# Kernel optimization log

Measured on AMD Instinct MI355X. Metric: run time of the kernel, lower is better.

Reference implementation:

```python
import jax, jax.numpy as jnp
import numpy as np

B, L, D, H = 2, 2048, 1024, 16
HD = D // H
EPS = 1e-6

def _rms(x, w):
    return x * jax.lax.rsqrt(jnp.mean(x * x, axis=-1, keepdims=True) + EPS) * w

def _lin(x, w, b=None):
    y = x @ w.T
    return y if b is None else y + b

def setup_inputs() -> dict:
    key = jax.random.key(0)
    ks = jax.random.split(key, 16)
    def w(i, shape, s=0.02):
        return jax.random.normal(ks[i], shape, dtype=jnp.float32) * s
    return dict(
        z=jax.random.normal(ks[0], (B, L, D), dtype=jnp.float32),
        connection=jax.random.normal(ks[1], (B, L, D), dtype=jnp.float32),
        w_z=jnp.ones(D, jnp.float32), w_c=jnp.ones(D, jnp.float32), w_mlp=jnp.ones(D, jnp.float32),
        f_w1=w(2, (2 * D, D)), f_b1=jnp.zeros(2 * D, jnp.float32),
        f_w2=w(3, (D, 2 * D)), f_b2=jnp.zeros(D, jnp.float32),
        g_w1=w(4, (D, 2 * D)), g_b1=jnp.zeros(D, jnp.float32),
        g_w2=w(5, (D, D)), g_b2=jnp.zeros(D, jnp.float32),
        dt=jnp.float32(0.1),
        q_w=w(6, (D, 2 * D)), k_w=w(7, (D, 2 * D)), v_w=w(8, (D, D)), o_w=w(9, (D, D)),
        temp=jnp.float32(1.0),
        cu_w1=w(10, (2 * D, 3 * D)), cu_b1=jnp.zeros(2 * D, jnp.float32),
        cu_w2=w(11, (D, 2 * D)), cu_b2=jnp.zeros(D, jnp.float32),
        m_w1=w(12, (4 * D, D)), m_b1=jnp.zeros(4 * D, jnp.float32),
        m_w2=w(13, (D, 4 * D)), m_b2=jnp.zeros(D, jnp.float32),
    )

def reference(z, connection, w_z, w_c, w_mlp,
              f_w1, f_b1, f_w2, f_b2, g_w1, g_b1, g_w2, g_b2, dt,
              q_w, k_w, v_w, o_w, temp,
              cu_w1, cu_b1, cu_w2, cu_b2,
              m_w1, m_b1, m_w2, m_b2):
    z_before = z
    zn = _rms(z, w_z)
    cn = _rms(connection, w_c)

    # covariant vector field: dz = dt * (F(zn) + gamma(cat(cn, F(zn))))
    dz_local = _lin(jax.nn.silu(_lin(zn, f_w1, f_b1)), f_w2, f_b2)
    corr = _lin(jnp.tanh(_lin(jnp.concatenate([cn, dz_local], -1), g_w1, g_b1)), g_w2, g_b2)
    dz = dt * (dz_local + corr)

    # covariant sigmoid attention
    zc = jnp.concatenate([zn, cn], -1)                       # [B,L,2D]
    Q = _lin(zc, q_w).reshape(B, L, H, HD).transpose(0, 2, 1, 3)  # bhld
    K = _lin(zc, k_w).reshape(B, L, H, HD).transpose(0, 2, 1, 3)
    V = _lin(zn, v_w).reshape(B, L, H, HD).transpose(0, 2, 1, 3)
    scores = jnp.einsum('bhld,bhmd->bhlm', Q, K) * (HD ** -0.5) * temp
    rel = jax.nn.sigmoid(scores)
    rel_sum = jnp.clip(jnp.sum(rel, -1, keepdims=True), 1.0, None)
    attn = jnp.einsum('bhlm,bhmd->bhld', rel, V) / rel_sum
    ctx = _lin(attn.transpose(0, 2, 1, 3).reshape(B, L, D), o_w)

    z1 = z + dz + ctx

    # connection update
    delta = _lin(jax.nn.silu(_lin(jnp.concatenate([connection, z1, dz], -1), cu_w1, cu_b1)), cu_w2, cu_b2)
    conn_new = connection + delta

    # MLP block
    z2 = z1 + _lin(jax.nn.silu(_lin(_rms(z1, w_mlp), m_w1, m_b1)), m_w2, m_b2)
    return (z2, conn_new, z_before)
```

## Files before the change

kernel.cpp:

```cpp
#include <hip/hip_runtime.h>


typedef unsigned short u16;
typedef __attribute__((ext_vector_type(8))) short short8;
typedef __attribute__((ext_vector_type(8))) unsigned short us8;
typedef __attribute__((ext_vector_type(4))) float f32x4;
typedef __attribute__((ext_vector_type(4))) unsigned short us4;
typedef __attribute__((ext_vector_type(2))) unsigned int u32x2;

__device__ __forceinline__ float b2f(u16 u) {
    union { unsigned u; float f; } c; c.u = ((unsigned)u) << 16; return c.f;
}
__device__ __forceinline__ u16 f2b(float f) {
    union { float f; unsigned u; } c; c.f = f;
    unsigned x = c.u;
    unsigned r = (x + 0x7fffu + ((x >> 16) & 1u)) >> 16;
    return (u16)r;
}
__device__ __forceinline__ float fast_rcp(float x) {
    return __builtin_amdgcn_rcpf(x);
}
__device__ __forceinline__ unsigned cvt_pk_bf16(float a, float b) {
    unsigned r;
    asm("v_cvt_pk_bf16_f32 %0, %1, %2" : "=v"(r) : "v"(a), "v"(b));
    return r;
}

__device__ __forceinline__ void async_copy16(const u16* g, u16* l) {
    __builtin_amdgcn_global_load_lds(
        (const __attribute__((address_space(1))) unsigned int*)(g),
        (__attribute__((address_space(3))) unsigned int*)(l), 16, 0, 0);
}

__global__ __launch_bounds__(256) void cvt_k(const float* __restrict__ s,
                                             u16* __restrict__ d, int n) {
    int i = (blockIdx.x * 256 + threadIdx.x) * 4;
    if (i >= n) return;
    f32x4 v = *(const f32x4*)(s + i);
    us4 o;
#pragma unroll
    for (int k = 0; k < 4; k++) o[k] = f2b(v[k]);
    *(us4*)(d + i) = o;
}

__global__ __launch_bounds__(256) void rmsf_k(const float* __restrict__ x,
                                              const float* __restrict__ w,
                                              u16* __restrict__ y,
                                              float* __restrict__ cp, int D) {
    int n = blockIdx.x;
    const float* xr = x + (size_t)n * D;
    int i0 = threadIdx.x << 2;
    f32x4 v = *(const f32x4*)(xr + i0);
    if (cp) *(f32x4*)(cp + (size_t)n * D + i0) = v;
    float s = v[0] * v[0] + v[1] * v[1] + v[2] * v[2] + v[3] * v[3];
#pragma unroll
    for (int m = 32; m >= 1; m >>= 1) s += __shfl_xor(s, m, 64);
    __shared__ float red[4];
    if ((threadIdx.x & 63) == 0) red[threadIdx.x >> 6] = s;
    __syncthreads();
    float tot = red[0] + red[1] + red[2] + red[3];
    float scale = rsqrtf(tot / (float)D + 1e-6f);
    f32x4 wv = *(const f32x4*)(w + i0);
    us4 o;
#pragma unroll
    for (int k = 0; k < 4; k++) o[k] = f2b(v[k] * scale * wv[k]);
    *(us4*)(y + (size_t)n * D + i0) = o;
}

__global__ __launch_bounds__(256) void rmsb_k(const u16* __restrict__ x,
                                              const float* __restrict__ w,
                                              u16* __restrict__ y, int D) {
    int n = blockIdx.x;
    const u16* xr = x + (size_t)n * D;
    int i0 = threadIdx.x << 2;
    us4 xv = *(const us4*)(xr + i0);
    float v[4]; float s = 0.f;
#pragma unroll
    for (int k = 0; k < 4; k++) { v[k] = b2f(xv[k]); s += v[k] * v[k]; }
#pragma unroll
    for (int m = 32; m >= 1; m >>= 1) s += __shfl_xor(s, m, 64);
    __shared__ float red[4];
    if ((threadIdx.x & 63) == 0) red[threadIdx.x >> 6] = s;
    __syncthreads();
    float tot = red[0] + red[1] + red[2] + red[3];
    float scale = rsqrtf(tot / (float)D + 1e-6f);
    f32x4 wv = *(const f32x4*)(w + i0);
    us4 o;
#pragma unroll
    for (int k = 0; k < 4; k++) o[k] = f2b(v[k] * scale * wv[k]);
    *(us4*)(y + (size_t)n * D + i0) = o;
}

template <int BN, int NSEG>
__global__ __launch_bounds__(256) void gemm_t(const u16* __restrict__ A0,
                                              const u16* __restrict__ A1,
                                              const u16* __restrict__ A2,
                                              const u16* __restrict__ W,
                                              const float* __restrict__ bias,
                                              u16* __restrict__ C,
                                              int K, int O, int act, int mode) {
    constexpr int NJ = BN / 32;
    constexpr int WN = BN / 2;
    __shared__ u16 Asm[2][128 * 64];
    __shared__ u16 Bsm[2][BN * 64];

    const int tid = threadIdx.x;
    const int wid = tid >> 6, lane = tid & 63;
    const int l15 = lane & 15, quad = lane >> 4;
    const int lsw = l15 & 7;
    const int row0 = blockIdx.y * 128, col0 = blockIdx.x * BN;
    const int wm = (wid >> 1) << 6, wn = (wid & 1) * WN;

    const int rb = tid >> 3;
    const int gg = ((tid & 7) ^ (rb & 7)) << 3;
    const int sA = (NSEG == 1) ? K : 1024;
    const size_t aoff = (size_t)(row0 + rb) * sA + gg;
    const size_t boff = (size_t)(col0 + rb) * K + gg;
    const int ldsb = wid << 9;

    f32x4 acc[4][NJ];
#pragma unroll
    for (int i = 0; i < 4; i++)
#pragma unroll
        for (int j = 0; j < NJ; j++) acc[i][j] = (f32x4){0.f, 0.f, 0.f, 0.f};

    auto stage = [&](int buf, int kof) {
        const u16* Ab; int kcol;
        if constexpr (NSEG == 1) { Ab = A0; kcol = kof; }
        else {
            int seg = kof >> 10;
            Ab = (seg == 0) ? A0 : ((NSEG == 3 && seg == 2) ? A2 : A1);
            kcol = kof & 1023;
        }
        const u16* as = Ab + aoff + kcol;
        const u16* bs = W + boff + kof;
#pragma unroll
        for (int i = 0; i < 4; i++)
            async_copy16(as + (size_t)(32 * i) * sA, &Asm[buf][(i << 11) + ldsb]);
#pragma unroll
        for (int i = 0; i < BN / 32; i++)
            async_copy16(bs + (size_t)(32 * i) * K, &Bsm[buf][(i << 11) + ldsb]);
    };

    const int nk = K >> 6;
    stage(0, 0);
    __syncthreads();
    for (int kk = 0; kk < nk; kk++) {
        int cur = kk & 1;
        if (kk + 1 < nk) stage(1 - cur, (kk + 1) << 6);
        const u16* Ab = Asm[cur];
        const u16* Bb = Bsm[cur];
#pragma unroll
        for (int h = 0; h < 2; h++) {
            const int gq = (((h << 2) + quad) ^ lsw) << 3;
            short8 af[4], bf[NJ];
#pragma unroll
            for (int i = 0; i < 4; i++)
                af[i] = *(const short8*)&Ab[(wm + i * 16 + l15) * 64 + gq];
#pragma unroll
            for (int j = 0; j < NJ; j++)
                bf[j] = *(const short8*)&Bb[(wn + j * 16 + l15) * 64 + gq];
#pragma unroll
            for (int i = 0; i < 4; i++)
#pragma unroll
                for (int j = 0; j < NJ; j++)
                    acc[i][j] = __builtin_amdgcn_mfma_f32_16x16x32_bf16(af[i], bf[j], acc[i][j], 0, 0, 0);
        }
        __syncthreads();
    }

    if (mode == 0) {
#pragma unroll
        for (int j = 0; j < NJ; j++) {
            int col = col0 + wn + j * 16 + l15;
            float bb = bias ? bias[col] : 0.f;
#pragma unroll
            for (int i = 0; i < 4; i++) {
                int rowb = row0 + wm + i * 16 + (quad << 2);
#pragma unroll
                for (int g = 0; g < 4; g++) {
                    float v = acc[i][j][g] + bb;
                    if (act == 1) {
                        v = v * fast_rcp(1.f + __expf(-v));
                    } else if (act == 2) {
                        float t = __expf(v * 2.f);
                        v = 1.f - 2.f * fast_rcp(1.f + t);
                    }
                    C[(size_t)(rowb + g) * O + col] = f2b(v);
                }
            }
        }
    } else {
#pragma unroll
        for (int j = 0; j < NJ; j++) {
            int col = col0 + wn + j * 16 + l15;
            int h = col >> 6, d = col & 63;
#pragma unroll
            for (int i = 0; i < 4; i++) {
                int rowb = row0 + wm + i * 16 + (quad << 2);
                int bb_ = rowb >> 11;
                int tok = rowb & 2047;
                us4 pk;
#pragma unroll
                for (int g = 0; g < 4; g++) pk[g] = f2b(acc[i][j][g]);
                *(us4*)&C[(size_t)(((bb_ << 4) + h) * 64 + d) * 2048 + tok] = pk;
            }
        }
    }
}

__global__ __launch_bounds__(256) void attn_k(const u16* __restrict__ QK,
                                              const u16* __restrict__ VT,
                                              const float* __restrict__ temp_p,
                                              u16* __restrict__ Oa) {
    const int L = 2048, D = 1024, SQ = 2048;
    __shared__ u16 Ks[2][64 * 64];
    __shared__ u16 Vs[2][64 * 64];
    __shared__ u16 plds[4][16 * 72];

    const int tid = threadIdx.x;
    const int w = tid >> 6, lane = tid & 63;
    const int l15 = lane & 15, quad = lane >> 4;
    const int bh = blockIdx.x >> 4;
    const int qb0 = (blockIdx.x & 15) << 7;
    const int b = bh >> 4, h = bh & 15;
    const float nsc2 = -0.125f * temp_p[0] * 1.44269504f;

    short8 aq[2][2];
#pragma unroll
    for (int qt = 0; qt < 2; qt++) {
        size_t row = (size_t)(b * L + qb0 + w * 32 + qt * 16 + l15) * SQ + h * 64;
#pragma unroll
        for (int hf = 0; hf < 2; hf++)
            aq[qt][hf] = *(const short8*)(QK + row + hf * 32 + quad * 8);
    }

    const u16* Kbase = QK + 1024 + (size_t)(b * L) * SQ + h * 64;
    const u16* VTb   = VT + (size_t)bh * 64 * L;

    const int i0 = tid, i1 = tid + 256;
    const int r0 = i0 >> 3, g0 = (i0 & 7) ^ (r0 & 7);
    const int r1 = i1 >> 3, g1 = (i1 & 7) ^ (r1 & 7);
    const u16* kS0 = Kbase + (size_t)r0 * SQ + g0 * 8;
    const u16* kS1 = Kbase + (size_t)r1 * SQ + g1 * 8;
    const u16* vS0 = VTb + (size_t)r0 * L + g0 * 8;
    const u16* vS1 = VTb + (size_t)r1 * L + g1 * 8;

    auto stage = [&](int buf, int mc) {
        async_copy16(kS0 + (size_t)mc * SQ, &Ks[buf][w << 9]);
        async_copy16(kS1 + (size_t)mc * SQ, &Ks[buf][2048 + (w << 9)]);
        async_copy16(vS0 + mc, &Vs[buf][w << 9]);
        async_copy16(vS1 + mc, &Vs[buf][2048 + (w << 9)]);
    };

    f32x4 acc[2][4];
#pragma unroll
    for (int i = 0; i < 2; i++)
#pragma unroll
        for (int j = 0; j < 4; j++) acc[i][j] = (f32x4){0.f, 0.f, 0.f, 0.f};
    float rs[2] = {0.f, 0.f};
    u16* P = plds[w];
    const int lsw = l15 & 7;

    stage(0, 0);
    __syncthreads();
    for (int it = 0; it < 32; it++) {
        int cur = it & 1;
        if (it < 31) stage(1 - cur, (it + 1) << 6);
        const u16* Kt = Ks[cur];
        const u16* Vt = Vs[cur];
#pragma unroll
        for (int qt = 0; qt < 2; qt++) {
#pragma unroll
            for (int ks = 0; ks < 4; ks++) {
                f32x4 s = (f32x4){0.f, 0.f, 0.f, 0.f};
#pragma unroll
                for (int hf = 0; hf < 2; hf++) {
                    int slot = ((ks * 16 + l15) * 8 + ((hf * 4 + quad) ^ lsw)) * 8;
                    short8 bk = *(const short8*)&Kt[slot];
                    s = __builtin_amdgcn_mfma_f32_16x16x32_bf16(bk, aq[qt][hf], s, 0, 0, 0);
                }
                float p0 = fast_rcp(1.f + __builtin_amdgcn_exp2f(s[0] * nsc2));
                float p1 = fast_rcp(1.f + __builtin_amdgcn_exp2f(s[1] * nsc2));
                float p2 = fast_rcp(1.f + __builtin_amdgcn_exp2f(s[2] * nsc2));
                float p3 = fast_rcp(1.f + __builtin_amdgcn_exp2f(s[3] * nsc2));
                rs[qt] += (p0 + p1) + (p2 + p3);
                u32x2 pk2;
                pk2[0] = cvt_pk_bf16(p0, p1);
                pk2[1] = cvt_pk_bf16(p2, p3);
                *(u32x2*)&P[l15 * 72 + ks * 16 + (quad << 2)] = pk2;
            }
#pragma unroll
            for (int kh = 0; kh < 2; kh++) {
                short8 ap = *(const short8*)&P[l15 * 72 + kh * 32 + quad * 8];
#pragma unroll
                for (int dt = 0; dt < 4; dt++) {
                    int slot = ((dt * 16 + l15) * 8 + ((kh * 4 + quad) ^ lsw)) * 8;
                    short8 bv = *(const short8*)&Vt[slot];
                    acc[qt][dt] = __builtin_amdgcn_mfma_f32_16x16x32_bf16(ap, bv, acc[qt][dt], 0, 0, 0);
                }
            }
        }
        __syncthreads();
    }

#pragma unroll
    for (int qt = 0; qt < 2; qt++) {
        rs[qt] += __shfl_xor(rs[qt], 16, 64);
        rs[qt] += __shfl_xor(rs[qt], 32, 64);
    }

#pragma unroll
    for (int qt = 0; qt < 2; qt++) {
        u16* orow = Oa + (size_t)(b * L + qb0 + w * 32 + qt * 16) * D + h * 64;
#pragma unroll
        for (int g = 0; g < 4; g++) {
            int row = quad * 4 + g;
            float denom = __shfl(rs[qt], row, 64);
            float rd = fast_rcp(fmaxf(denom, 1.0f));
#pragma unroll
            for (int dt = 0; dt < 4; dt++)
                orow[(size_t)row * D + dt * 16 + l15] = f2b(acc[qt][dt][g] * rd);
        }
    }
}

__global__ void dz_k(u16* __restrict__ d, const u16* __restrict__ a,
                     const u16* __restrict__ b, const float* __restrict__ dtp, int n) {
    int i = (blockIdx.x * 256 + threadIdx.x) * 8;
    if (i >= n) return;
    float dt = dtp[0];
    us8 va = *(const us8*)(a + i), vb = *(const us8*)(b + i);
    us8 o;
#pragma unroll
    for (int k = 0; k < 8; k++) o[k] = f2b(dt * (b2f(va[k]) + b2f(vb[k])));
    *(us8*)(d + i) = o;
}

__global__ void z1_k(u16* __restrict__ d, const float* __restrict__ z,
                     const u16* __restrict__ dz, const u16* __restrict__ ctx, int n) {
    int i = (blockIdx.x * 256 + threadIdx.x) * 8;
    if (i >= n) return;
    f32x4 z0 = *(const f32x4*)(z + i), z4 = *(const f32x4*)(z + i + 4);
    us8 vd = *(const us8*)(dz + i), vc = *(const us8*)(ctx + i);
    us8 o;
#pragma unroll
    for (int k = 0; k < 4; k++) {
        o[k]     = f2b(z0[k] + b2f(vd[k])     + b2f(vc[k]));
        o[k + 4] = f2b(z4[k] + b2f(vd[k + 4]) + b2f(vc[k + 4]));
    }
    *(us8*)(d + i) = o;
}

__global__ void connew_k(float* __restrict__ d, const float* __restrict__ conn,
                         const u16* __restrict__ delta, int n) {
    int i = (blockIdx.x * 256 + threadIdx.x) * 8;
    if (i >= n) return;
    f32x4 c0 = *(const f32x4*)(conn + i), c4 = *(const f32x4*)(conn + i + 4);
    us8 vd = *(const us8*)(delta + i);
    f32x4 o0, o4;
#pragma unroll
    for (int k = 0; k < 4; k++) {
        o0[k] = c0[k] + b2f(vd[k]);
        o4[k] = c4[k] + b2f(vd[k + 4]);
    }
    *(f32x4*)(d + i) = o0;
    *(f32x4*)(d + i + 4) = o4;
}

__global__ void z2_k(float* __restrict__ d, const u16* __restrict__ z1,
                     const u16* __restrict__ mf, int n) {
    int i = (blockIdx.x * 256 + threadIdx.x) * 8;
    if (i >= n) return;
    us8 va = *(const us8*)(z1 + i), vb = *(const us8*)(mf + i);
    f32x4 o0, o4;
#pragma unroll
    for (int k = 0; k < 4; k++) {
        o0[k] = b2f(va[k]) + b2f(vb[k]);
        o4[k] = b2f(va[k + 4]) + b2f(vb[k + 4]);
    }
    *(f32x4*)(d + i) = o0;
    *(f32x4*)(d + i + 4) = o4;
}

extern "C" void kernel_launch(void* const* d_in, const int* in_sizes, int n_in,
                              void* d_out, int out_size, void* d_ws, size_t ws_size,
                              hipStream_t stream) {
    const int B = 2, L = 2048, D = 1024, H = 16, N = B * L;
    const float* z      = (const float*)d_in[0];
    const float* conn   = (const float*)d_in[1];
    const float* w_z    = (const float*)d_in[2];
    const float* w_c    = (const float*)d_in[3];
    const float* w_mlp  = (const float*)d_in[4];
    const float* f_w1   = (const float*)d_in[5];
    const float* f_b1   = (const float*)d_in[6];
    const float* f_w2   = (const float*)d_in[7];
    const float* f_b2   = (const float*)d_in[8];
    const float* g_w1   = (const float*)d_in[9];
    const float* g_b1   = (const float*)d_in[10];
    const float* g_w2   = (const float*)d_in[11];
    const float* g_b2   = (const float*)d_in[12];
    const float* dt_p   = (const float*)d_in[13];
    const float* q_w    = (const float*)d_in[14];
    const float* k_w    = (const float*)d_in[15];
    const float* v_w    = (const float*)d_in[16];
    const float* o_w    = (const float*)d_in[17];
    const float* temp_p = (const float*)d_in[18];
    const float* cu_w1  = (const float*)d_in[19];
    const float* cu_b1  = (const float*)d_in[20];
    const float* cu_w2  = (const float*)d_in[21];
    const float* cu_b2  = (const float*)d_in[22];
    const float* m_w1   = (const float*)d_in[23];
    const float* m_b1   = (const float*)d_in[24];
    const float* m_w2   = (const float*)d_in[25];
    const float* m_b2   = (const float*)d_in[26];

    float* out = (float*)d_out;
    u16* ws  = (u16*)d_ws;
    const size_t U = (size_t)N * D;

    u16* zn    = ws + 0 * U;
    u16* cn    = ws + 1 * U;
    u16* h1    = ws + 2 * U;
    u16* dzl   = ws + 4 * U;
    u16* gh    = ws + 5 * U;
    u16* corr  = ws + 6 * U;
    u16* dz    = ws + 7 * U;
    u16* connb = ws + 8 * U;
    u16* QK    = ws + 2 * U;
    u16* VT    = ws + 4 * U;
    u16* attnb = ws + 1 * U;
    u16* ctx   = ws + 4 * U;
    u16* z1    = ws + 5 * U;
    u16* cu_h  = ws + 2 * U;
    u16* delta = ws + 1 * U;
    u16* z1n   = ws + 0 * U;
    u16* mh    = ws + 1 * U;
    u16* mf    = ws + 6 * U;

    u16* wb = ws + 9 * U;
    u16* bf_w1  = wb + 0;
    u16* bf_w2  = wb + 2 * 1024 * 1024;
    u16* bg_w1  = wb + 4 * 1024 * 1024;
    u16* bg_w2  = wb + 6 * 1024 * 1024;
    u16* bqk_w  = wb + 7 * 1024 * 1024;
    u16* bv_w   = wb + 11 * 1024 * 1024;
    u16* bo_w   = wb + 12 * 1024 * 1024;
    u16* bcu_w1 = wb + 13 * 1024 * 1024;
    u16* bcu_w2 = wb + 19 * 1024 * 1024;
    u16* bm_w1  = wb + 21 * 1024 * 1024;
    u16* bm_w2  = wb + 25 * 1024 * 1024;

    auto cvt = [&](const float* s, u16* d, int n) {
        cvt_k<<<n / 1024, 256, 0, stream>>>(s, d, n);
    };
    cvt(f_w1, bf_w1, 2 * D * D);   cvt(f_w2, bf_w2, 2 * D * D);
    cvt(g_w1, bg_w1, 2 * D * D);   cvt(g_w2, bg_w2, D * D);
    cvt(q_w, bqk_w, 2 * D * D);    cvt(k_w, bqk_w + 2 * D * D, 2 * D * D);
    cvt(v_w, bv_w, D * D);         cvt(o_w, bo_w, D * D);
    cvt(cu_w1, bcu_w1, 6 * D * D); cvt(cu_w2, bcu_w2, 2 * D * D);
    cvt(m_w1, bm_w1, 4 * D * D);   cvt(m_w2, bm_w2, 4 * D * D);
    cvt(conn, connb, N * D);

    const int EW8 = (N * D / 8 + 255) / 256;
    auto gemm = [&](const u16* A, const u16* W, const float* bias, u16* C,
                    int K, int O, int act, int mode = 0) {
        if (O == 1024) {
            dim3 grid(16, 32);
            gemm_t<64, 1><<<grid, 256, 0, stream>>>(A, nullptr, nullptr, W, bias, C, K, O, act, mode);
        } else {
            dim3 grid(O / 128, 32);
            gemm_t<128, 1><<<grid, 256, 0, stream>>>(A, nullptr, nullptr, W, bias, C, K, O, act, mode);
        }
    };

    rmsf_k<<<N, 256, 0, stream>>>(z, w_z, zn, out + 2 * U, D);
    rmsf_k<<<N, 256, 0, stream>>>(conn, w_c, cn, nullptr, D);

    gemm(zn, bf_w1, f_b1, h1, D, 2 * D, 1);
    gemm(h1, bf_w2, f_b2, dzl, 2 * D, D, 0);
    gemm_t<64, 2><<<dim3(16, 32), 256, 0, stream>>>(
        cn, dzl, nullptr, bg_w1, g_b1, gh, 2 * D, D, 2, 0);
    gemm(gh, bg_w2, g_b2, corr, D, D, 0);
    dz_k<<<EW8, 256, 0, stream>>>(dz, dzl, corr, dt_p, N * D);

    gemm_t<128, 2><<<dim3(16, 32), 256, 0, stream>>>(
        zn, cn, nullptr, bqk_w, nullptr, QK, 2 * D, 2 * D, 0, 0);
    gemm(zn, bv_w, nullptr, VT, D, D, 0, 1);
    attn_k<<<B * H * L / 128, 256, 0, stream>>>(QK, VT, temp_p, attnb);
    gemm(attnb, bo_w, nullptr, ctx, D, D, 0);

    z1_k<<<EW8, 256, 0, stream>>>(z1, z, dz, ctx, N * D);

    gemm_t<128, 3><<<dim3(16, 32), 256, 0, stream>>>(
        connb, z1, dz, bcu_w1, cu_b1, cu_h, 3 * D, 2 * D, 1, 0);
    gemm(cu_h, bcu_w2, cu_b2, delta, 2 * D, D, 0);
    connew_k<<<EW8, 256, 0, stream>>>(out + U, conn, delta, N * D);

    rmsb_k<<<N, 256, 0, stream>>>(z1, w_mlp, z1n, D);
    gemm(z1n, bm_w1, m_b1, mh, D, 4 * D, 1);
    gemm(mh, bm_w2, m_b2, mf, 4 * D, D, 0);
    z2_k<<<EW8, 256, 0, stream>>>(out, z1, mf, N * D);
}
```

Measured before the change: 749.9 us.

## Load attention K/V directly to registers and remap workgroup IDs for XCD locality

Result: slower. 767.3 us (+2.3%).

```diff
diff --git a/kernel.cpp b/kernel.cpp
--- a/kernel.cpp
+++ b/kernel.cpp
@@ -108,7 +108,13 @@
     const int wid = tid >> 6, lane = tid & 63;
     const int l15 = lane & 15, quad = lane >> 4;
     const int lsw = l15 & 7;
-    const int row0 = blockIdx.y * 128, col0 = blockIdx.x * BN;
+
+    const int nwg = gridDim.x * gridDim.y;
+    int id = blockIdx.y * gridDim.x + blockIdx.x;
+    id = (id & 7) * (nwg >> 3) + (id >> 3);
+    const int bx = id % gridDim.x, by = id / gridDim.x;
+
+    const int row0 = by * 128, col0 = bx * BN;
     const int wm = (wid >> 1) << 6, wn = (wid & 1) * WN;
 
     const int rb = tid >> 3;
@@ -200,10 +206,10 @@
                 int rowb = row0 + wm + i * 16 + (quad << 2);
                 int bb_ = rowb >> 11;
                 int tok = rowb & 2047;
-                us4 pk;
-#pragma unroll
-                for (int g = 0; g < 4; g++) pk[g] = f2b(acc[i][j][g]);
-                *(us4*)&C[(size_t)(((bb_ << 4) + h) * 64 + d) * 2048 + tok] = pk;
+                u32x2 pk2;
+                pk2[0] = cvt_pk_bf16(acc[i][j][0], acc[i][j][1]);
+                pk2[1] = cvt_pk_bf16(acc[i][j][2], acc[i][j][3]);
+                *(u32x2*)&C[(size_t)(((bb_ << 4) + h) * 64 + d) * 2048 + tok] = pk2;
             }
         }
     }
@@ -214,15 +220,15 @@
                                               const float* __restrict__ temp_p,
                                               u16* __restrict__ Oa) {
     const int L = 2048, D = 1024, SQ = 2048;
-    __shared__ u16 Ks[2][64 * 64];
-    __shared__ u16 Vs[2][64 * 64];
     __shared__ u16 plds[4][16 * 72];
 
     const int tid = threadIdx.x;
     const int w = tid >> 6, lane = tid & 63;
     const int l15 = lane & 15, quad = lane >> 4;
-    const int bh = blockIdx.x >> 4;
-    const int qb0 = (blockIdx.x & 15) << 7;
+    int id = blockIdx.x;
+    id = (id & 7) * 64 + (id >> 3);
+    const int bh = id >> 4;
+    const int qb0 = (id & 15) << 7;
     const int b = bh >> 4, h = bh & 15;
     const float nsc2 = -0.125f * temp_p[0] * 1.44269504f;
 
@@ -235,23 +241,8 @@
             aq[qt][hf] = *(const short8*)(QK + row + hf * 32 + quad * 8);
     }
 
-    const u16* Kbase = QK + 1024 + (size_t)(b * L) * SQ + h * 64;
-    const u16* VTb   = VT + (size_t)bh * 64 * L;
-
-    const int i0 = tid, i1 = tid + 256;
-    const int r0 = i0 >> 3, g0 = (i0 & 7) ^ (r0 & 7);
-    const int r1 = i1 >> 3, g1 = (i1 & 7) ^ (r1 & 7);
-    const u16* kS0 = Kbase + (size_t)r0 * SQ + g0 * 8;
-    const u16* kS1 = Kbase + (size_t)r1 * SQ + g1 * 8;
-    const u16* vS0 = VTb + (size_t)r0 * L + g0 * 8;
-    const u16* vS1 = VTb + (size_t)r1 * L + g1 * 8;
-
-    auto stage = [&](int buf, int mc) {
-        async_copy16(kS0 + (size_t)mc * SQ, &Ks[buf][w << 9]);
-        async_copy16(kS1 + (size_t)mc * SQ, &Ks[buf][2048 + (w << 9)]);
-        async_copy16(vS0 + mc, &Vs[buf][w << 9]);
-        async_copy16(vS1 + mc, &Vs[buf][2048 + (w << 9)]);
-    };
+    const u16* Kb = QK + 1024 + (size_t)(b * L) * SQ + h * 64;
+    const u16* Vb = VT + (size_t)bh * 64 * L;
 
     f32x4 acc[2][4];
 #pragma unroll
@@ -260,26 +251,32 @@
         for (int j = 0; j < 4; j++) acc[i][j] = (f32x4){0.f, 0.f, 0.f, 0.f};
     float rs[2] = {0.f, 0.f};
     u16* P = plds[w];
-    const int lsw = l15 & 7;
-
-    stage(0, 0);
-    __syncthreads();
+
     for (int it = 0; it < 32; it++) {
-        int cur = it & 1;
-        if (it < 31) stage(1 - cur, (it + 1) << 6);
-        const u16* Kt = Ks[cur];
-        const u16* Vt = Vs[cur];
+        const int key0 = it << 6;
+        short8 bk[4][2], bv[4][2];
+#pragma unroll
+        for (int ks = 0; ks < 4; ks++) {
+            const u16* kr = Kb + (size_t)(key0 + ks * 16 + l15) * SQ + quad * 8;
+#pragma unroll
+            for (int hf = 0; hf < 2; hf++)
+                bk[ks][hf] = *(const short8*)(kr + hf * 32);
+        }
+#pragma unroll
+        for (int dt = 0; dt < 4; dt++) {
+            const u16* vr = Vb + (size_t)(dt * 16 + l15) * L + key0 + quad * 8;
+#pragma unroll
+            for (int kh = 0; kh < 2; kh++)
+                bv[dt][kh] = *(const short8*)(vr + kh * 32);
+        }
 #pragma unroll
         for (int qt = 0; qt < 2; qt++) {
 #pragma unroll
             for (int ks = 0; ks < 4; ks++) {
                 f32x4 s = (f32x4){0.f, 0.f, 0.f, 0.f};
 #pragma unroll
-                for (int hf = 0; hf < 2; hf++) {
-                    int slot = ((ks * 16 + l15) * 8 + ((hf * 4 + quad) ^ lsw)) * 8;
-                    short8 bk = *(const short8*)&Kt[slot];
-                    s = __builtin_amdgcn_mfma_f32_16x16x32_bf16(bk, aq[qt][hf], s, 0, 0, 0);
-                }
+                for (int hf = 0; hf < 2; hf++)
+                    s = __builtin_amdgcn_mfma_f32_16x16x32_bf16(bk[ks][hf], aq[qt][hf], s, 0, 0, 0);
                 float p0 = fast_rcp(1.f + __builtin_amdgcn_exp2f(s[0] * nsc2));
                 float p1 = fast_rcp(1.f + __builtin_amdgcn_exp2f(s[1] * nsc2));
                 float p2 = fast_rcp(1.f + __builtin_amdgcn_exp2f(s[2] * nsc2));
@@ -294,14 +291,10 @@
             for (int kh = 0; kh < 2; kh++) {
                 short8 ap = *(const short8*)&P[l15 * 72 + kh * 32 + quad * 8];
 #pragma unroll
-                for (int dt = 0; dt < 4; dt++) {
-                    int slot = ((dt * 16 + l15) * 8 + ((kh * 4 + quad) ^ lsw)) * 8;
-                    short8 bv = *(const short8*)&Vt[slot];
-                    acc[qt][dt] = __builtin_amdgcn_mfma_f32_16x16x32_bf16(ap, bv, acc[qt][dt], 0, 0, 0);
-                }
+                for (int dt = 0; dt < 4; dt++)
+                    acc[qt][dt] = __builtin_amdgcn_mfma_f32_16x16x32_bf16(ap, bv[dt][kh], acc[qt][dt], 0, 0, 0);
             }
         }
-        __syncthreads();
     }
 
 #pragma unroll
```
